# Kernel tuning notes

Hardware: AMD Instinct MI355X
Metric: run time of the kernel (lower is better)

The kernel has to match this reference:

```python
import jax, jax.numpy as jnp
import numpy as np
from jax import lax

B = 512          # scoring batch size
NC = 10          # n_classes
N_LAB = 256      # int(B * plb), plb = 0.5 (labeled indices are the first N_LAB)
TOL = 1e-3       # gtg_t
MAX_ITER = 30    # gtg_i
INTERM = 128
CH = [64, 128, 256, 512]
SZ = [32, 16, 8, 4]
EMB = 512


def setup_inputs() -> dict:
    key = jax.random.key(0)
    ks = jax.random.split(key, 16)
    inp = {}
    for i, (c, s) in enumerate(zip(CH, SZ)):
        inp["feat%d" % i] = jax.random.normal(ks[i], (B, c, s, s), jnp.float32)
        inp["conv_w%d" % i] = jax.random.normal(ks[4 + i], (c, c, 3, 3), jnp.float32) * 0.05
        inp["conv_b%d" % i] = jnp.zeros((c,), jnp.float32)
        inp["bn_g%d" % i] = jnp.ones((c,), jnp.float32)
        inp["bn_b%d" % i] = jnp.zeros((c,), jnp.float32)
        inp["lin_w%d" % i] = jax.random.normal(ks[8 + i], (INTERM, c), jnp.float32) * 0.05
        inp["lin_b%d" % i] = jnp.zeros((INTERM,), jnp.float32)
    inp["fin_w"] = jax.random.normal(ks[12], (1, 4 * INTERM), jnp.float32) * 0.05
    inp["fin_b"] = jnp.zeros((1,), jnp.float32)
    inp["embedds"] = jax.random.normal(ks[13], (B, EMB), jnp.float32)
    inp["labels"] = jax.random.randint(ks[14], (B,), 0, NC)
    return inp


def _branch(x, cw, cb, g, b, lw, lb):
    # Conv3x3(same) -> BatchNorm (train mode, batch stats, eps=1e-5) -> ReLU -> GAP -> Linear -> ReLU
    y = lax.conv_general_dilated(x, cw, (1, 1), 'SAME',
                                 dimension_numbers=('NCHW', 'OIHW', 'NCHW')) + cb[None, :, None, None]
    m = y.mean(axis=(0, 2, 3), keepdims=True)
    v = ((y - m) ** 2).mean(axis=(0, 2, 3), keepdims=True)  # biased variance (train-mode BN)
    y = jax.nn.relu(g[None, :, None, None] * (y - m) * lax.rsqrt(v + 1e-5) + b[None, :, None, None])
    y = y.mean(axis=(2, 3))  # AvgPool2d(feature_size) == global average pool -> [B, C]
    return jax.nn.relu(y @ lw.T + lb)


def _gtg(E, labels):
    # get_A_e_d: pairwise euclidean distances clamped to [0.1, 1.0]
    sq = jnp.sum(E * E, axis=1)
    d2 = jnp.maximum(sq[:, None] + sq[None, :] - 2.0 * (E @ E.T), 0.0)
    A0 = jnp.clip(jnp.sqrt(d2), 0.1, 1.0)
    # rbf kernel: 7th nearest neighbor (ascending for 'e_d') gives per-sample sigma
    seventh = E[jnp.argsort(A0, axis=1)[:, 6]]
    sig = jnp.clip(jnp.sqrt(jnp.sum((E - seventh) ** 2, axis=1)), 0.1, 1.0)
    A = jnp.clip(jnp.exp(-(A0 ** 2) / (sig[:, None] * sig[None, :])), 0.0, 1.0)
    # threshold strategy 'mean' with AM_function == 'e_d': A = where(A > mean(A), 1, A)
    A = jnp.where(A > A.mean(), 1.0, A)
    # AM_strategy 'mixed' with 'e_d': flip only the labeled x labeled block
    A = A.at[:N_LAB, :N_LAB].set(1.0 - A[:N_LAB, :N_LAB])
    # get_X: one-hot for labeled (first N_LAB), uniform 1/NC for unlabeled
    X0 = jnp.concatenate([jax.nn.one_hot(labels[:N_LAB], NC, dtype=jnp.float32),
                          jnp.full((B - N_LAB, NC), 1.0 / NC, jnp.float32)], axis=0)
    hist0 = jnp.zeros((B, MAX_ITER), jnp.float32)

    def cond(c):
        return (c[3] > TOL) & (c[2] < MAX_ITER)

    def body(c):
        X, h, i, _ = c
        Xn = X * (A @ X)
        Xn = Xn / jnp.sum(Xn, axis=1, keepdims=True)
        ent = -jnp.sum(jnp.where(Xn > 0, Xn * jnp.log(Xn), 0.0), axis=1)
        h = lax.dynamic_update_slice(h, ent[:, None], (0, i))
        return (Xn, h, i + 1, jnp.linalg.norm(Xn - X))

    X, h, _, _ = lax.while_loop(cond, body, (X0, hist0, jnp.int32(0), jnp.float32(jnp.inf)))
    return h.mean(axis=1), X  # ent_strategy == 'mean'


def reference(feat0, feat1, feat2, feat3,
              conv_w0, conv_b0, bn_g0, bn_b0, lin_w0, lin_b0,
              conv_w1, conv_b1, bn_g1, bn_b1, lin_w1, lin_b1,
              conv_w2, conv_b2, bn_g2, bn_b2, lin_w2, lin_b2,
              conv_w3, conv_b3, bn_g3, bn_b3, lin_w3, lin_b3,
              fin_w, fin_b, embedds, labels):
    o0 = _branch(feat0, conv_w0, conv_b0, bn_g0, bn_b0, lin_w0, lin_b0)
    o1 = _branch(feat1, conv_w1, conv_b1, bn_g1, bn_b1, lin_w1, lin_b1)
    o2 = _branch(feat2, conv_w2, conv_b2, bn_g2, bn_b2, lin_w2, lin_b2)
    o3 = _branch(feat3, conv_w3, conv_b3, bn_g3, bn_b3, lin_w3, lin_b3)
    y_pred = (jnp.concatenate([o0, o1, o2, o3], axis=1) @ fin_w.T + fin_b)[:, 0]
    y_true, X = _gtg(embedds, labels)
    labeled_mask = jnp.arange(B) < N_LAB
    return (y_pred, y_true, X, labeled_mask)
```

## Files before the change

kernel.cpp:

```cpp
#include <hip/hip_runtime.h>
#include <hip/hip_bf16.h>
#include <math.h>

static constexpr int kNC = 10;
static constexpr int kNLab = 256;
static constexpr int kMaxIter = 30;

using short8 = __attribute__((ext_vector_type(8))) short;
using f32x4  = __attribute__((ext_vector_type(4))) float;

__device__ __forceinline__ unsigned short f2bf(float f) {
  unsigned int u = __float_as_uint(f);
  u += 0x7FFFu + ((u >> 16) & 1u);
  return (unsigned short)(u >> 16);
}
__device__ __forceinline__ float bf2f(unsigned short u) {
  return __uint_as_float(((unsigned int)u) << 16);
}

template <int C, int S>
__global__ __launch_bounds__(256) void xpack_kernel(const float* __restrict__ x,
                                                    unsigned short* __restrict__ xp) {
  __shared__ float t[C][S + 1];
  const int n = blockIdx.x / S, h = blockIdx.x % S;
  const float* src = x + (size_t)n * C * S * S;
  for (int e = threadIdx.x; e < C * S; e += 256) {
    int c = e / S, w = e % S;
    t[c][w] = src[((size_t)c * S + h) * S + w];
  }
  __syncthreads();
  unsigned short* dst = xp + ((size_t)(n * S + h) * S) * C;
  for (int e = threadIdx.x; e < C * S; e += 256) {
    int w = e / C, c = e % C;
    dst[(size_t)w * C + c] = f2bf(t[c][w]);
  }
}

__global__ void wpack_all(const float* __restrict__ w0, const float* __restrict__ w1,
                          const float* __restrict__ w2, const float* __restrict__ w3,
                          unsigned short* __restrict__ wpk) {
  int idx = blockIdx.x * 256 + threadIdx.x;
  if (idx >= 3133440) return;
  const float* w; int C, off;
  if (idx < 36864)        { w = w0; C = 64;  off = 0; }
  else if (idx < 184320)  { w = w1; C = 128; off = 36864; }
  else if (idx < 774144)  { w = w2; C = 256; off = 184320; }
  else                    { w = w3; C = 512; off = 774144; }
  int e = idx - off;
  int CO16T = C / 16, CIK = C / 32;
  int e8 = e & 7, l = (e >> 3) & 63;
  int rest = e >> 9;
  int co16 = rest % CO16T;
  int rest2 = rest / CO16T;
  int cik = rest2 % CIK, tap = rest2 / CIK;
  int co = co16 * 16 + (l & 15);
  int ci = cik * 32 + (l >> 4) * 8 + e8;
  wpk[idx] = f2bf(w[((size_t)co * C + ci) * 9 + tap]);
}

template <int C, int S, int NI, int NR, int WV, int BF, int MODE>
__global__ __launch_bounds__(WV * 64)
void conv_mfma(const unsigned short* __restrict__ xp, const unsigned short* __restrict__ wpk,
               const float* __restrict__ bias, unsigned short* __restrict__ y,
               float* __restrict__ psum, float* __restrict__ psq, int npart, int partBase,
               const float* __restrict__ scale, const float* __restrict__ shift,
               float* __restrict__ pp, int pxGlobalBase) {
  constexpr int SS = S * S;
  constexpr int PXB = NI * NR * S;
  constexpr int TPB = WV * 64;
  constexpr int HR = NR + 2, HC = S + 2;
  constexpr int CIK = C / 32, CO16T = C / 16;
  constexpr int UNITS = NI * HR * HC * 4;
  constexpr int NU = (UNITS + TPB - 1) / TPB;
  static_assert(WV * BF * 16 == PXB, "wave px mismatch");
  static_assert(MODE != 2 || BF == 4, "MODE2 assumes 64px/wave");
  __shared__ __align__(16) char xs[NI * HR * HC * 80];

  const int tid = threadIdx.x;
  const int wv = tid >> 6, l = tid & 63, l15 = l & 15, l4 = l >> 4;
  const int coblk = blockIdx.y;
  const int co_base = coblk * 64;
  const int pxb = blockIdx.x * PXB;
  const int n_t = pxb / SS;
  const int r0 = (pxb % SS) / S;

  int pxoff[BF];
#pragma unroll
  for (int bf = 0; bf < BF; ++bf) {
    int pxloc = wv * (BF * 16) + bf * 16 + l15;
    int ii = pxloc / (NR * S);
    int rr = (pxloc % (NR * S)) / S;
    int cc = pxloc % S;
    pxoff[bf] = ((ii * HR + rr) * HC + cc) * 80 + l4 * 16;
  }

  f32x4 acc[4][BF];
#pragma unroll
  for (int a = 0; a < 4; ++a)
#pragma unroll
    for (int b = 0; b < BF; ++b) acc[a][b] = (f32x4){0.f, 0.f, 0.f, 0.f};

  uint4 vreg[NU];
  auto loadU = [&](int cik) {
#pragma unroll
    for (int k = 0; k < NU; ++k) {
      int u = tid + k * TPB;
      uint4 v = {0u, 0u, 0u, 0u};
      if (u < UNITS) {
        int k16 = u & 3;
        int t = u >> 2;
        int hc = t % HC;
        int t2 = t / HC;
        int hr = t2 % HR;
        int ii = t2 / HR;
        int row = r0 + hr - 1, col = hc - 1;
        if (row >= 0 && row < S && col >= 0 && col < S)
          v = *(const uint4*)(xp + ((size_t)((n_t + ii) * S + row) * S + col) * C + cik * 32 + k16 * 8);
      }
      vreg[k] = v;
    }
  };

  loadU(0);
  for (int cik = 0; cik < CIK; ++cik) {
    __syncthreads();
#pragma unroll
    for (int k = 0; k < NU; ++k) {
      int u = tid + k * TPB;
      if (u < UNITS) *(uint4*)(xs + (u >> 2) * 80 + (u & 3) * 16) = vreg[k];
    }
    __syncthreads();
    if (cik + 1 < CIK) loadU(cik + 1);
#pragma unroll
    for (int tap = 0; tap < 9; ++tap) {
      const int tapoff = ((tap / 3) * HC + (tap % 3)) * 80;
      short8 wf[4], xf[BF];
#pragma unroll
      for (int af = 0; af < 4; ++af)
        wf[af] = *(const short8*)(wpk + ((size_t)((tap * CIK + cik) * CO16T + coblk * 4 + af) * 64 + l) * 8);
#pragma unroll
      for (int bf = 0; bf < BF; ++bf)
        xf[bf] = *(const short8*)(xs + pxoff[bf] + tapoff);
#pragma unroll
      for (int af = 0; af < 4; ++af)
#pragma unroll
        for (int bf = 0; bf < BF; ++bf)
          acc[af][bf] = __builtin_amdgcn_mfma_f32_16x16x32_bf16(wf[af], xf[bf], acc[af][bf], 0, 0, 0);
    }
  }

#pragma unroll
  for (int af = 0; af < 4; ++af) {
    const int co0 = co_base + af * 16 + l4 * 4;
    float4 bv = *(const float4*)(bias + co0);
    float s[4] = {0.f, 0.f, 0.f, 0.f}, q[4] = {0.f, 0.f, 0.f, 0.f};
    float4 sc4, sh4;
    if (MODE == 2) {
      sc4 = *(const float4*)(scale + co0);
      sh4 = *(const float4*)(shift + co0);
    }
#pragma unroll
    for (int bf = 0; bf < BF; ++bf) {
      float o[4];
#pragma unroll
      for (int r = 0; r < 4; ++r) o[r] = acc[af][bf][r] + ((const float*)&bv)[r];
      if (MODE == 0) {
        ushort4 pk;
        pk.x = f2bf(o[0]); pk.y = f2bf(o[1]); pk.z = f2bf(o[2]); pk.w = f2bf(o[3]);
        size_t px = (size_t)(pxb + wv * (BF * 16) + bf * 16 + l15);
        *(ushort4*)(y + px * C + co0) = pk;
      }
      if (MODE == 2) {
#pragma unroll
        for (int r = 0; r < 4; ++r)
          s[r] += fmaxf(fmaf(((const float*)&sc4)[r], o[r], ((const float*)&sh4)[r]), 0.f);
      } else {
#pragma unroll
        for (int r = 0; r < 4; ++r) { s[r] += o[r]; q[r] += o[r] * o[r]; }
      }
    }
#pragma unroll
    for (int m = 1; m < 16; m <<= 1) {
#pragma unroll
      for (int r = 0; r < 4; ++r) {
        s[r] += __shfl_xor(s[r], m);
        if (MODE != 2) q[r] += __shfl_xor(q[r], m);
      }
    }
    if (l15 == 0) {
      if (MODE == 2) {
        int n = (pxGlobalBase + pxb) / SS;
        int qw = ((pxGlobalBase + pxb) % SS) / 64 + wv;
#pragma unroll
        for (int r = 0; r < 4; ++r)
          pp[((size_t)(n * C + co0 + r)) * 16 + qw] = s[r];
      } else {
        int part = partBase + blockIdx.x * WV + wv;
#pragma unroll
        for (int r = 0; r < 4; ++r) {
          psum[(size_t)(co0 + r) * npart + part] = s[r];
          psq[(size_t)(co0 + r) * npart + part] = q[r];
        }
      }
    }
  }
}

__global__ __launch_bounds__(256)
void stats2_kernel(const float* __restrict__ psum, const float* __restrict__ psq,
                   const float* __restrict__ g, const float* __restrict__ bb,
                   float* __restrict__ scale, float* __restrict__ shift,
                   int npart, float invN) {
  int c = blockIdx.x;
  __shared__ float rs[256], rq[256];
  float s = 0.f, q = 0.f;
  for (int p = threadIdx.x; p < npart; p += 256) {
    s += psum[(size_t)c * npart + p];
    q += psq[(size_t)c * npart + p];
  }
  rs[threadIdx.x] = s; rq[threadIdx.x] = q;
  __syncthreads();
  for (int st = 128; st; st >>= 1) {
    if (threadIdx.x < st) { rs[threadIdx.x] += rs[threadIdx.x + st]; rq[threadIdx.x] += rq[threadIdx.x + st]; }
    __syncthreads();
  }
  if (threadIdx.x == 0) {
    float m = rs[0] * invN;
    float v = rq[0] * invN - m * m;
    float sc = g[c] / sqrtf(v + 1e-5f);
    scale[c] = sc;
    shift[c] = bb[c] - m * sc;
  }
}

template <int C, int S>
__global__ __launch_bounds__(256)
void pool_lin(const unsigned short* __restrict__ y, const float* __restrict__ scale,
              const float* __restrict__ shift, const float* __restrict__ lw,
              const float* __restrict__ lb, float* __restrict__ oc, int brOff) {
  constexpr int SS = S * S;
  int n = blockIdx.x;
  const unsigned short* yr = y + (size_t)n * SS * C;
  __shared__ float pl[C];
  if (C >= 256) {
    for (int co = threadIdx.x; co < C; co += 256) {
      float sc = scale[co], sh = shift[co], s = 0.f;
      for (int p = 0; p < SS; ++p) s += fmaxf(fmaf(sc, bf2f(yr[(size_t)p * C + co]), sh), 0.f);
      pl[co] = s * (1.f / SS);
    }
  } else {
    constexpr int G = 256 / C;
    int co = threadIdx.x % C;
    int sl = threadIdx.x / C;
    float sc = scale[co], sh = shift[co], s = 0.f;
    for (int p = sl; p < SS; p += G) s += fmaxf(fmaf(sc, bf2f(yr[(size_t)p * C + co]), sh), 0.f);
    __shared__ float red[256];
    red[threadIdx.x] = s;
    __syncthreads();
    if (threadIdx.x < C) {
      float t = 0.f;
      for (int gg = 0; gg < G; ++gg) t += red[gg * C + co];
      pl[co] = t * (1.f / SS);
    }
  }
  __syncthreads();
  if (threadIdx.x < 128) {
    int j = threadIdx.x;
    const float* wr = lw + (size_t)j * C;
    float s = 0.f;
    for (int t = 0; t < C; ++t) s = fmaf(pl[t], wr[t], s);
    s += lb[j];
    oc[n * 512 + brOff + j] = fmaxf(s, 0.f);
  }
}

__global__ void poolfin_kernel(const float* __restrict__ pp, float* __restrict__ pooled) {
  int i = blockIdx.x * 256 + threadIdx.x;
  if (i >= 512 * 64) return;
  float s = 0.f;
  for (int qn = 0; qn < 16; ++qn) s += pp[(size_t)i * 16 + qn];
  pooled[i] = s * (1.f / 1024.f);
}

__global__ void lin_kernel(const float* __restrict__ pooled, const float* __restrict__ lw,
                           const float* __restrict__ lb, float* __restrict__ oc,
                           int C, int brOff) {
  int idx = blockIdx.x * 256 + threadIdx.x;
  if (idx >= 512 * 128) return;
  int j = idx & 127, n = idx >> 7;
  const float4* pr = (const float4*)(pooled + (size_t)n * C);
  const float4* wr = (const float4*)(lw + (size_t)j * C);
  float s = 0.f;
  for (int t = 0; t < C / 4; ++t) {
    float4 a = pr[t], b = wr[t];
    s += a.x * b.x + a.y * b.y + a.z * b.z + a.w * b.w;
  }
  s += lb[j];
  oc[n * 512 + brOff + j] = fmaxf(s, 0.f);
}

__global__ void ypred_kernel(const float* __restrict__ oc, const float* __restrict__ fw,
                             const float* __restrict__ fb, float* __restrict__ out) {
  int wv = threadIdx.x >> 6, l = threadIdx.x & 63;
  int n = blockIdx.x * 4 + wv;
  float s = 0.f;
  for (int k = l; k < 512; k += 64) s += oc[n * 512 + k] * fw[k];
#pragma unroll
  for (int m = 32; m; m >>= 1) s += __shfl_down(s, m);
  if (l == 0) out[n] = s + fb[0];
}

__global__ void sqnorm_kernel(const float* __restrict__ E, float* __restrict__ sq) {
  int wv = threadIdx.x >> 6, l = threadIdx.x & 63;
  int n = blockIdx.x * 4 + wv;
  const float* row = E + (size_t)n * 512;
  float s = 0.f;
  for (int k = l; k < 512; k += 64) { float v = row[k]; s += v * v; }
#pragma unroll
  for (int m = 32; m; m >>= 1) s += __shfl_down(s, m);
  if (l == 0) sq[n] = s;
}

__global__ __launch_bounds__(256) void a0_kernel(const float* __restrict__ E,
                                                 const float* __restrict__ sq,
                                                 float* __restrict__ A0) {
  int bi = blockIdx.x / 32, bj = blockIdx.x % 32;
  int ti = threadIdx.x % 16, tj = threadIdx.x / 16;
  __shared__ float Ei[16][68], Ej[16][68];
  float acc = 0.f;
  for (int k0 = 0; k0 < 512; k0 += 64) {
    for (int e = threadIdx.x; e < 1024; e += 256) {
      int rr = e >> 6, cc = e & 63;
      Ei[rr][cc] = E[(size_t)(bi * 16 + rr) * 512 + k0 + cc];
      Ej[rr][cc] = E[(size_t)(bj * 16 + rr) * 512 + k0 + cc];
    }
    __syncthreads();
#pragma unroll 16
    for (int kk = 0; kk < 64; ++kk) acc = fmaf(Ei[tj][kk], Ej[ti][kk], acc);
    __syncthreads();
  }
  int i = bi * 16 + tj, j = bj * 16 + ti;
  float d2 = fmaxf(sq[i] + sq[j] - 2.f * acc, 0.f);
  A0[(size_t)i * 512 + j] = fminf(fmaxf(sqrtf(d2), 0.1f), 1.0f);
}

__global__ void seventh_kernel(const float* __restrict__ A0, int* __restrict__ idx7) {
  int i = blockIdx.x * 256 + threadIdx.x;
  if (i >= 512) return;
  float v[7]; int ix[7];
#pragma unroll
  for (int t = 0; t < 7; ++t) { v[t] = 3.4e38f; ix[t] = 0; }
  const float* row = A0 + (size_t)i * 512;
  for (int j = 0; j < 512; ++j) {
    float a = row[j];
    if (a < v[6]) {
      int pos = 6;
      while (pos > 0 && a < v[pos - 1]) { v[pos] = v[pos - 1]; ix[pos] = ix[pos - 1]; --pos; }
      v[pos] = a; ix[pos] = j;
    }
  }
  idx7[i] = ix[6];
}

__global__ void sig_kernel(const float* __restrict__ E, const int* __restrict__ idx7,
                           float* __restrict__ sig) {
  int wv = threadIdx.x >> 6, l = threadIdx.x & 63;
  int n = blockIdx.x * 4 + wv;
  const float* r1 = E + (size_t)n * 512;
  const float* r2 = E + (size_t)idx7[n] * 512;
  float s = 0.f;
  for (int k = l; k < 512; k += 64) { float d = r1[k] - r2[k]; s += d * d; }
#pragma unroll
  for (int m = 32; m; m >>= 1) s += __shfl_down(s, m);
  if (l == 0) sig[n] = fminf(fmaxf(sqrtf(s), 0.1f), 1.0f);
}

__global__ void aexp_kernel(const float* __restrict__ A0, const float* __restrict__ sig,
                            float* __restrict__ A, float* __restrict__ part) {
  int t = blockIdx.x * 256 + threadIdx.x;
  int base = t * 4;
  int i = base >> 9, j0 = base & 511;
  float si = sig[i];
  float4 a = *(const float4*)(A0 + base);
  float4 o;
  o.x = fminf(fmaxf(expf(-a.x * a.x / (si * sig[j0 + 0])), 0.f), 1.f);
  o.y = fminf(fmaxf(expf(-a.y * a.y / (si * sig[j0 + 1])), 0.f), 1.f);
  o.z = fminf(fmaxf(expf(-a.z * a.z / (si * sig[j0 + 2])), 0.f), 1.f);
  o.w = fminf(fmaxf(expf(-a.w * a.w / (si * sig[j0 + 3])), 0.f), 1.f);
  *(float4*)(A + base) = o;
  float lsum = o.x + o.y + o.z + o.w;
#pragma unroll
  for (int m = 32; m; m >>= 1) lsum += __shfl_down(lsum, m);
  __shared__ float sred[4];
  if ((threadIdx.x & 63) == 0) sred[threadIdx.x >> 6] = lsum;
  __syncthreads();
  if (threadIdx.x == 0) part[blockIdx.x] = sred[0] + sred[1] + sred[2] + sred[3];
}

__global__ void meanred_kernel(const float* __restrict__ part, float* __restrict__ meanA) {
  if (threadIdx.x == 0 && blockIdx.x == 0) {
    float s = 0.f;
    for (int p = 0; p < 256; ++p) s += part[p];
    meanA[0] = s * (1.0f / 262144.0f);
  }
}

__global__ void thresh_kernel(float* __restrict__ A, const float* __restrict__ meanA) {
  int t = blockIdx.x * 256 + threadIdx.x;
  int base = t * 4;
  int i = base >> 9, j0 = base & 511;
  float m = meanA[0];
  float4 v = *(const float4*)(A + base);
  v.x = v.x > m ? 1.f : v.x;
  v.y = v.y > m ? 1.f : v.y;
  v.z = v.z > m ? 1.f : v.z;
  v.w = v.w > m ? 1.f : v.w;
  if (i < kNLab && j0 < kNLab) {
    v.x = 1.f - v.x; v.y = 1.f - v.y; v.z = 1.f - v.z; v.w = 1.f - v.w;
  }
  *(float4*)(A + base) = v;
}

__global__ __launch_bounds__(1024)
void gtg1(const float* __restrict__ A, const int* __restrict__ labels,
          float* __restrict__ out) {
  const int tid = threadIdx.x;
  const int w = tid >> 6, l = tid & 63;
  const int rc = w & 3, g = w >> 2;
  const int i = rc * 64 + l;
  __shared__ float Xs[256][12];
  __shared__ float Ls[256][12];
  __shared__ float axred[4][256][12];
  __shared__ float dredw[4];
  __shared__ int labs[256];

  if (tid < 256) labs[tid] = labels[tid];
  for (int e = tid; e < 256 * 12; e += 1024)
    (&Xs[0][0])[e] = ((e % 12) < 10) ? 0.1f : 0.f;
  __syncthreads();

  const float* Ar = A + (size_t)(256 + i) * 512;
  float areg[64];
#pragma unroll
  for (int q = 0; q < 16; ++q) {
    float4 v = *(const float4*)(Ar + 256 + g * 64 + q * 4);
    areg[q * 4 + 0] = v.x; areg[q * 4 + 1] = v.y;
    areg[q * 4 + 2] = v.z; areg[q * 4 + 3] = v.w;
  }
  {
    float lp[10];
#pragma unroll
    for (int c = 0; c < 10; ++c) lp[c] = 0.f;
    for (int q = 0; q < 16; ++q) {
      float4 v = *(const float4*)(Ar + g * 64 + q * 4);
      float av[4] = {v.x, v.y, v.z, v.w};
#pragma unroll
      for (int k = 0; k < 4; ++k) {
        int lab = labs[g * 64 + q * 4 + k];
#pragma unroll
        for (int c = 0; c < 10; ++c) lp[c] += (lab == c) ? av[k] : 0.f;
      }
    }
    *(float4*)&axred[g][i][0] = make_float4(lp[0], lp[1], lp[2], lp[3]);
    *(float4*)&axred[g][i][4] = make_float4(lp[4], lp[5], lp[6], lp[7]);
    *(float2*)&axred[g][i][8] = make_float2(lp[8], lp[9]);
  }
  __syncthreads();
  if (g == 0) {
    float s[10];
#pragma unroll
    for (int c = 0; c < 10; ++c) s[c] = 0.f;
#pragma unroll
    for (int q = 0; q < 4; ++q) {
      float4 a0 = *(const float4*)&axred[q][i][0];
      float4 a1 = *(const float4*)&axred[q][i][4];
      float2 a2 = *(const float2*)&axred[q][i][8];
      s[0] += a0.x; s[1] += a0.y; s[2] += a0.z; s[3] += a0.w;
      s[4] += a1.x; s[5] += a1.y; s[6] += a1.z; s[7] += a1.w;
      s[8] += a2.x; s[9] += a2.y;
    }
    *(float4*)&Ls[i][0] = make_float4(s[0], s[1], s[2], s[3]);
    *(float4*)&Ls[i][4] = make_float4(s[4], s[5], s[6], s[7]);
    *(float2*)&Ls[i][8] = make_float2(s[8], s[9]);
  }
  __syncthreads();

  float entsum = 0.f;
  float nrm2 = 1e30f;
  for (int it = 0; it < kMaxIter; ++it) {
    if (it > 0 && sqrtf(nrm2) <= 0.001f) break;
    float ax[10];
#pragma unroll
    for (int c = 0; c < 10; ++c) ax[c] = 0.f;
#pragma unroll
    for (int jj = 0; jj < 64; ++jj) {
      const int j = g * 64 + jj;
      float4 x0 = *(const float4*)&Xs[j][0];
      float4 x1 = *(const float4*)&Xs[j][4];
      float2 x2 = *(const float2*)&Xs[j][8];
      float a = areg[jj];
      ax[0] = fmaf(a, x0.x, ax[0]); ax[1] = fmaf(a, x0.y, ax[1]);
      ax[2] = fmaf(a, x0.z, ax[2]); ax[3] = fmaf(a, x0.w, ax[3]);
      ax[4] = fmaf(a, x1.x, ax[4]); ax[5] = fmaf(a, x1.y, ax[5]);
      ax[6] = fmaf(a, x1.z, ax[6]); ax[7] = fmaf(a, x1.w, ax[7]);
      ax[8] = fmaf(a, x2.x, ax[8]); ax[9] = fmaf(a, x2.y, ax[9]);
    }
    *(float4*)&axred[g][i][0] = make_float4(ax[0], ax[1], ax[2], ax[3]);
    *(float4*)&axred[g][i][4] = make_float4(ax[4], ax[5], ax[6], ax[7]);
    *(float2*)&axred[g][i][8] = make_float2(ax[8], ax[9]);
    __syncthreads();
    if (g == 0) {
      float s[10];
#pragma unroll
      for (int c = 0; c < 10; ++c) s[c] = Ls[i][c];
#pragma unroll
      for (int q = 0; q < 4; ++q) {
        float4 a0 = *(const float4*)&axred[q][i][0];
        float4 a1 = *(const float4*)&axred[q][i][4];
        float2 a2 = *(const float2*)&axred[q][i][8];
        s[0] += a0.x; s[1] += a0.y; s[2] += a0.z; s[3] += a0.w;
        s[4] += a1.x; s[5] += a1.y; s[6] += a1.z; s[7] += a1.w;
        s[8] += a2.x; s[9] += a2.y;
      }
      float xn[10], ssum = 0.f;
#pragma unroll
      for (int c = 0; c < 10; ++c) { xn[c] = Xs[i][c] * s[c]; ssum += xn[c]; }
      float ent = 0.f, dp = 0.f;
#pragma unroll
      for (int c = 0; c < 10; ++c) {
        float xv = xn[c] / ssum;
        if (xv > 0.f) ent -= xv * logf(xv);
        float d = xv - Xs[i][c];
        dp += d * d;
        Xs[i][c] = xv;
      }
      entsum += ent;
#pragma unroll
      for (int m = 1; m < 64; m <<= 1) dp += __shfl_xor(dp, m);
      if (l == 0) dredw[rc] = dp;
    }
    __syncthreads();
    nrm2 = dredw[0] + dredw[1] + dredw[2] + dredw[3];
  }

  if (g == 0) out[512 + 256 + i] = entsum * (1.0f / 30.0f);
  for (int e = tid; e < 256; e += 1024) {
    out[512 + e] = 0.f;
    out[6144 + e] = 1.f;
    out[6144 + 256 + e] = 0.f;
  }
  for (int e = tid; e < 2560; e += 1024) {
    int r = e / 10, c = e % 10;
    out[1024 + e] = (labs[r] == c) ? 1.f : 0.f;
    out[1024 + 2560 + e] = Xs[r][c];
  }
}

extern "C" void kernel_launch(void* const* d_in, const int* in_sizes, int n_in,
                              void* d_out, int out_size, void* d_ws, size_t ws_size,
                              hipStream_t stream) {
  (void)in_sizes; (void)n_in; (void)out_size;

  const float* feat[4]; const float* cw[4]; const float* cbp[4];
  const float* bg[4]; const float* bbp[4]; const float* lw[4]; const float* lbp[4];
  for (int b = 0; b < 4; ++b) {
    int base = b * 7;
    feat[b] = (const float*)d_in[base + 0];
    cw[b]  = (const float*)d_in[base + 1];
    cbp[b] = (const float*)d_in[base + 2];
    bg[b]  = (const float*)d_in[base + 3];
    bbp[b] = (const float*)d_in[base + 4];
    lw[b]  = (const float*)d_in[base + 5];
    lbp[b] = (const float*)d_in[base + 6];
  }
  const float* finw = (const float*)d_in[28];
  const float* finb = (const float*)d_in[29];
  const float* emb  = (const float*)d_in[30];
  const int* labels = (const int*)d_in[31];
  float* out = (float*)d_out;

  float* wsf = (float*)d_ws;
  unsigned short* xpad = (unsigned short*)wsf;
  unsigned short* yP   = (unsigned short*)(wsf + 4194304);
  unsigned short* wpk  = (unsigned short*)(wsf + 12582912);
  size_t off = 14149632;
  float* psum = wsf + off; off += 524288;
  float* psq  = wsf + off; off += 524288;
  float* pp   = wsf + off; off += 524288;
  float* scale = wsf + off; off += 512;
  float* shift = wsf + off; off += 512;
  float* pooled = wsf + off; off += 491520;
  float* oc = wsf + off; off += 262144;
  float* sq = wsf + off; off += 512;
  float* A0 = wsf + off; off += 262144;
  float* Am = wsf + off; off += 262144;
  float* sig = wsf + off; off += 512;
  int* idx7 = (int*)(wsf + off); off += 512;
  float* meanPart = wsf + off; off += 256;
  float* meanA = wsf + off; off += 4;
  size_t yb0_off = off;
  unsigned short* yB0 = (unsigned short*)(wsf + yb0_off);
  const bool bigB0 = ws_size >= (yb0_off + 16777216) * sizeof(float);

  unsigned short* wpkB[4] = {wpk, wpk + 36864, wpk + 184320, wpk + 774144};

  wpack_all<<<(3133440 + 255) / 256, 256, 0, stream>>>(cw[0], cw[1], cw[2], cw[3], wpk);

  for (int c = 0; c < 2; ++c) {
    xpack_kernel<128, 16><<<256 * 16, 256, 0, stream>>>(feat[1] + (size_t)c * 8388608, xpad);
    conv_mfma<128, 16, 1, 8, 4, 2, 0><<<dim3(512, 2), 256, 0, stream>>>(
        xpad, wpkB[1], cbp[1], yP + (size_t)c * 8388608, psum, psq, 4096, c * 2048,
        nullptr, nullptr, nullptr, 0);
  }
  stats2_kernel<<<128, 256, 0, stream>>>(psum, psq, bg[1], bbp[1], scale, shift, 4096, 1.f / 131072.f);
  pool_lin<128, 16><<<512, 256, 0, stream>>>(yP, scale, shift, lw[1], lbp[1], oc, 128);

  xpack_kernel<256, 8><<<512 * 8, 256, 0, stream>>>(feat[2], xpad);
  conv_mfma<256, 8, 2, 8, 4, 2, 0><<<dim3(256, 4), 256, 0, stream>>>(
      xpad, wpkB[2], cbp[2], yP, psum, psq, 1024, 0, nullptr, nullptr, nullptr, 0);
  stats2_kernel<<<256, 256, 0, stream>>>(psum, psq, bg[2], bbp[2], scale, shift, 1024, 1.f / 32768.f);
  pool_lin<256, 8><<<512, 256, 0, stream>>>(yP, scale, shift, lw[2], lbp[2], oc, 256);

  xpack_kernel<512, 4><<<512 * 4, 256, 0, stream>>>(feat[3], xpad);
  conv_mfma<512, 4, 8, 4, 4, 2, 0><<<dim3(64, 8), 256, 0, stream>>>(
      xpad, wpkB[3], cbp[3], yP, psum, psq, 256, 0, nullptr, nullptr, nullptr, 0);
  stats2_kernel<<<512, 256, 0, stream>>>(psum, psq, bg[3], bbp[3], scale, shift, 256, 1.f / 8192.f);
  pool_lin<512, 4><<<512, 256, 0, stream>>>(yP, scale, shift, lw[3], lbp[3], oc, 384);

  if (bigB0) {
    for (int c = 0; c < 4; ++c) {
      xpack_kernel<64, 32><<<128 * 32, 256, 0, stream>>>(feat[0] + (size_t)c * 8388608, xpad);
      conv_mfma<64, 32, 1, 8, 4, 4, 0><<<dim3(512, 1), 256, 0, stream>>>(
          xpad, wpkB[0], cbp[0], yB0 + (size_t)c * 8388608, psum, psq, 8192, c * 2048,
          nullptr, nullptr, nullptr, 0);
    }
    stats2_kernel<<<64, 256, 0, stream>>>(psum, psq, bg[0], bbp[0], scale, shift, 8192, 1.f / 524288.f);
    pool_lin<64, 32><<<512, 256, 0, stream>>>(yB0, scale, shift, lw[0], lbp[0], oc, 0);
  } else {
    for (int c = 0; c < 4; ++c) {
      xpack_kernel<64, 32><<<128 * 32, 256, 0, stream>>>(feat[0] + (size_t)c * 8388608, xpad);
      conv_mfma<64, 32, 1, 8, 4, 4, 1><<<dim3(512, 1), 256, 0, stream>>>(
          xpad, wpkB[0], cbp[0], nullptr, psum, psq, 8192, c * 2048, nullptr, nullptr, nullptr, 0);
    }
    stats2_kernel<<<64, 256, 0, stream>>>(psum, psq, bg[0], bbp[0], scale, shift, 8192, 1.f / 524288.f);
    for (int c = 0; c < 4; ++c) {
      xpack_kernel<64, 32><<<128 * 32, 256, 0, stream>>>(feat[0] + (size_t)c * 8388608, xpad);
      conv_mfma<64, 32, 1, 8, 4, 4, 2><<<dim3(512, 1), 256, 0, stream>>>(
          xpad, wpkB[0], cbp[0], nullptr, nullptr, nullptr, 0, 0, scale, shift, pp, c * 131072);
    }
    poolfin_kernel<<<128, 256, 0, stream>>>(pp, pooled);
    lin_kernel<<<256, 256, 0, stream>>>(pooled, lw[0], lbp[0], oc, 64, 0);
  }

  ypred_kernel<<<128, 256, 0, stream>>>(oc, finw, finb, out);
  sqnorm_kernel<<<128, 256, 0, stream>>>(emb, sq);
  a0_kernel<<<1024, 256, 0, stream>>>(emb, sq, A0);
  seventh_kernel<<<2, 256, 0, stream>>>(A0, idx7);
  sig_kernel<<<128, 256, 0, stream>>>(emb, idx7, sig);
  aexp_kernel<<<256, 256, 0, stream>>>(A0, sig, Am, meanPart);
  meanred_kernel<<<1, 64, 0, stream>>>(meanPart, meanA);
  thresh_kernel<<<256, 256, 0, stream>>>(Am, meanA);

  gtg1<<<1, 1024, 0, stream>>>(Am, labels, out);
}
```

Before: 1.008 ms.

## Reduce GTG iteration partials with wave shuffles and double-buffer X state

```diff
diff --git a/kernel.cpp b/kernel.cpp
--- a/kernel.cpp
+++ b/kernel.cpp
@@ -421,83 +421,59 @@
   *(float4*)(A + base) = v;
 }
 
-__global__ __launch_bounds__(1024)
-void gtg1(const float* __restrict__ A, const int* __restrict__ labels,
+__global__ __launch_bounds__(1024, 4)
+void gtg2(const float* __restrict__ A, const int* __restrict__ labels,
           float* __restrict__ out) {
   const int tid = threadIdx.x;
   const int w = tid >> 6, l = tid & 63;
-  const int rc = w & 3, g = w >> 2;
-  const int i = rc * 64 + l;
-  __shared__ float Xs[256][12];
-  __shared__ float Ls[256][12];
-  __shared__ float axred[4][256][12];
-  __shared__ float dredw[4];
+  const int r = l & 15, g = l >> 4;
+  const int i = w * 16 + r;
+  __shared__ float Xs[2][256][12];
+  __shared__ float dredw[2][16];
   __shared__ int labs[256];
 
   if (tid < 256) labs[tid] = labels[tid];
   for (int e = tid; e < 256 * 12; e += 1024)
-    (&Xs[0][0])[e] = ((e % 12) < 10) ? 0.1f : 0.f;
+    (&Xs[0][0][0])[e] = ((e % 12) < 10) ? 0.1f : 0.f;
   __syncthreads();
 
-  const float* Ar = A + (size_t)(256 + i) * 512;
+  const float* Ar = A + (size_t)(256 + i) * 512 + g * 64;
   float areg[64];
 #pragma unroll
   for (int q = 0; q < 16; ++q) {
-    float4 v = *(const float4*)(Ar + 256 + g * 64 + q * 4);
+    float4 v = *(const float4*)(Ar + 256 + q * 4);
     areg[q * 4 + 0] = v.x; areg[q * 4 + 1] = v.y;
     areg[q * 4 + 2] = v.z; areg[q * 4 + 3] = v.w;
   }
-  {
-    float lp[10];
-#pragma unroll
-    for (int c = 0; c < 10; ++c) lp[c] = 0.f;
-    for (int q = 0; q < 16; ++q) {
-      float4 v = *(const float4*)(Ar + g * 64 + q * 4);
-      float av[4] = {v.x, v.y, v.z, v.w};
-#pragma unroll
-      for (int k = 0; k < 4; ++k) {
-        int lab = labs[g * 64 + q * 4 + k];
-#pragma unroll
-        for (int c = 0; c < 10; ++c) lp[c] += (lab == c) ? av[k] : 0.f;
-      }
-    }
-    *(float4*)&axred[g][i][0] = make_float4(lp[0], lp[1], lp[2], lp[3]);
-    *(float4*)&axred[g][i][4] = make_float4(lp[4], lp[5], lp[6], lp[7]);
-    *(float2*)&axred[g][i][8] = make_float2(lp[8], lp[9]);
-  }
-  __syncthreads();
-  if (g == 0) {
-    float s[10];
-#pragma unroll
-    for (int c = 0; c < 10; ++c) s[c] = 0.f;
-#pragma unroll
-    for (int q = 0; q < 4; ++q) {
-      float4 a0 = *(const float4*)&axred[q][i][0];
-      float4 a1 = *(const float4*)&axred[q][i][4];
-      float2 a2 = *(const float2*)&axred[q][i][8];
-      s[0] += a0.x; s[1] += a0.y; s[2] += a0.z; s[3] += a0.w;
-      s[4] += a1.x; s[5] += a1.y; s[6] += a1.z; s[7] += a1.w;
-      s[8] += a2.x; s[9] += a2.y;
-    }
-    *(float4*)&Ls[i][0] = make_float4(s[0], s[1], s[2], s[3]);
-    *(float4*)&Ls[i][4] = make_float4(s[4], s[5], s[6], s[7]);
-    *(float2*)&Ls[i][8] = make_float2(s[8], s[9]);
-  }
-  __syncthreads();
+  float lp[10];
+#pragma unroll
+  for (int c = 0; c < 10; ++c) lp[c] = 0.f;
+#pragma unroll
+  for (int q = 0; q < 16; ++q) {
+    float4 v = *(const float4*)(Ar + q * 4);
+    float av[4] = {v.x, v.y, v.z, v.w};
+#pragma unroll
+    for (int k = 0; k < 4; ++k) {
+      int lab = labs[g * 64 + q * 4 + k];
+#pragma unroll
+      for (int c = 0; c < 10; ++c) lp[c] += (lab == c) ? av[k] : 0.f;
+    }
+  }
 
   float entsum = 0.f;
   float nrm2 = 1e30f;
+  int cur = 0;
   for (int it = 0; it < kMaxIter; ++it) {
     if (it > 0 && sqrtf(nrm2) <= 0.001f) break;
     float ax[10];
 #pragma unroll
-    for (int c = 0; c < 10; ++c) ax[c] = 0.f;
+    for (int c = 0; c < 10; ++c) ax[c] = lp[c];
 #pragma unroll
     for (int jj = 0; jj < 64; ++jj) {
-      const int j = g * 64 + jj;
-      float4 x0 = *(const float4*)&Xs[j][0];
-      float4 x1 = *(const float4*)&Xs[j][4];
-      float2 x2 = *(const float2*)&Xs[j][8];
+      const float* xr = &Xs[cur][g * 64 + jj][0];
+      float4 x0 = *(const float4*)(xr);
+      float4 x1 = *(const float4*)(xr + 4);
+      float2 x2 = *(const float2*)(xr + 8);
       float a = areg[jj];
       ax[0] = fmaf(a, x0.x, ax[0]); ax[1] = fmaf(a, x0.y, ax[1]);
       ax[2] = fmaf(a, x0.z, ax[2]); ax[3] = fmaf(a, x0.w, ax[3]);
@@ -505,42 +481,36 @@
       ax[6] = fmaf(a, x1.z, ax[6]); ax[7] = fmaf(a, x1.w, ax[7]);
       ax[8] = fmaf(a, x2.x, ax[8]); ax[9] = fmaf(a, x2.y, ax[9]);
     }
-    *(float4*)&axred[g][i][0] = make_float4(ax[0], ax[1], ax[2], ax[3]);
-    *(float4*)&axred[g][i][4] = make_float4(ax[4], ax[5], ax[6], ax[7]);
-    *(float2*)&axred[g][i][8] = make_float2(ax[8], ax[9]);
-    __syncthreads();
+#pragma unroll
+    for (int c = 0; c < 10; ++c) {
+      ax[c] += __shfl_xor(ax[c], 16);
+      ax[c] += __shfl_xor(ax[c], 32);
+    }
+    float dp = 0.f;
     if (g == 0) {
-      float s[10];
-#pragma unroll
-      for (int c = 0; c < 10; ++c) s[c] = Ls[i][c];
-#pragma unroll
-      for (int q = 0; q < 4; ++q) {
-        float4 a0 = *(const float4*)&axred[q][i][0];
-        float4 a1 = *(const float4*)&axred[q][i][4];
-        float2 a2 = *(const float2*)&axred[q][i][8];
-        s[0] += a0.x; s[1] += a0.y; s[2] += a0.z; s[3] += a0.w;
-        s[4] += a1.x; s[5] += a1.y; s[6] += a1.z; s[7] += a1.w;
-        s[8] += a2.x; s[9] += a2.y;
-      }
       float xn[10], ssum = 0.f;
 #pragma unroll
-      for (int c = 0; c < 10; ++c) { xn[c] = Xs[i][c] * s[c]; ssum += xn[c]; }
-      float ent = 0.f, dp = 0.f;
+      for (int c = 0; c < 10; ++c) { xn[c] = Xs[cur][i][c] * ax[c]; ssum += xn[c]; }
+      float ent = 0.f;
 #pragma unroll
       for (int c = 0; c < 10; ++c) {
         float xv = xn[c] / ssum;
         if (xv > 0.f) ent -= xv * logf(xv);
-        float d = xv - Xs[i][c];
+        float d = xv - Xs[cur][i][c];
         dp += d * d;
-        Xs[i][c] = xv;
+        Xs[cur ^ 1][i][c] = xv;
       }
       entsum += ent;
-#pragma unroll
-      for (int m = 1; m < 64; m <<= 1) dp += __shfl_xor(dp, m);
-      if (l == 0) dredw[rc] = dp;
-    }
+    }
+#pragma unroll
+    for (int m = 1; m < 64; m <<= 1) dp += __shfl_xor(dp, m);
+    if (l == 0) dredw[it & 1][w] = dp;
     __syncthreads();
-    nrm2 = dredw[0] + dredw[1] + dredw[2] + dredw[3];
+    float s = 0.f;
+#pragma unroll
+    for (int q = 0; q < 16; ++q) s += dredw[it & 1][q];
+    nrm2 = s;
+    cur ^= 1;
   }
 
   if (g == 0) out[512 + 256 + i] = entsum * (1.0f / 30.0f);
@@ -550,9 +520,9 @@
     out[6144 + 256 + e] = 0.f;
   }
   for (int e = tid; e < 2560; e += 1024) {
-    int r = e / 10, c = e % 10;
-    out[1024 + e] = (labs[r] == c) ? 1.f : 0.f;
-    out[1024 + 2560 + e] = Xs[r][c];
+    int rr = e / 10, c = e % 10;
+    out[1024 + e] = (labs[rr] == c) ? 1.f : 0.f;
+    out[1024 + 2560 + e] = Xs[cur][rr][c];
   }
 }
 
@@ -661,5 +631,5 @@
   meanred_kernel<<<1, 64, 0, stream>>>(meanPart, meanA);
   thresh_kernel<<<256, 256, 0, stream>>>(Am, meanA);
 
-  gtg1<<<1, 1024, 0, stream>>>(Am, labels, out);
-}
+  gtg2<<<1, 1024, 0, stream>>>(Am, labels, out);
+}
```

Result: no change. 997.5 us (-1.0%).
